# Optimization experiments

Measured on AMD Instinct MI355X. Metric: run time of the kernel, lower is better.

Reference implementation:

```python
import jax, jax.numpy as jnp
import numpy as np

SEQ_LEN = 1000
IN_DIM = 100
POOL = SEQ_LEN // IN_DIM  # 10
HIDDEN = 64
OUT_DIM = 5
N_BASIS = 16
BATCH = 65536


def setup_inputs() -> dict:
    key = jax.random.key(0)
    k1, k2, k3 = jax.random.split(key, 3)
    x = jax.random.normal(k1, (BATCH, SEQ_LEN), dtype=jnp.float32)
    c1_mu = jax.random.normal(k2, (HIDDEN, IN_DIM, N_BASIS), dtype=jnp.float32) * 0.05
    c2_mu = jax.random.normal(k3, (OUT_DIM, HIDDEN, N_BASIS), dtype=jnp.float32) * 0.05
    centers = jnp.linspace(-3.0, 3.0, N_BASIS, dtype=jnp.float32)
    return {"x": x, "c1_mu": c1_mu, "c2_mu": c2_mu, "centers": centers}


def _norm(x):
    # torch .std() uses ddof=1 (unbiased)
    mu = jnp.mean(x, axis=1, keepdims=True)
    sd = jnp.std(x, axis=1, keepdims=True, ddof=1)
    return (x - mu) / (sd + 1e-6)


def _basis(x, centers):
    # x: [b, d] -> [b, d, n_basis]; RBF with fixed variance 0.36
    d = x[..., None] - centers
    return jnp.exp(-0.5 * d * d / 0.36)


def _kan(x, c, centers):
    B = _basis(x, centers)  # [b, i, n]
    return jnp.einsum('bin,oin->bo', B, c)


def reference(x, c1_mu, c2_mu, centers):
    b = x.shape[0]
    # unfold(1, pool, pool).mean(-1): non-overlapping average pooling
    x = x.reshape(b, IN_DIM, POOL).mean(-1)  # [b, 100]
    x = _norm(x)
    h = jnp.tanh(_kan(x, c1_mu, centers))  # [b, 64]
    h = _norm(h)
    out = _kan(h, c2_mu, centers)  # [b, 5]
    return out
```

## Files before the change

### kernel.cpp

```cpp
#include <hip/hip_runtime.h>
#include <hip/hip_bf16.h>


#define SEQ    1000
#define INDIM  100
#define HID    64
#define OUTD   5
#define ROWS   16
#define NTHR   128

typedef __bf16 v8bf __attribute__((ext_vector_type(8)));
typedef float  v4f  __attribute__((ext_vector_type(4)));

#define XSTR 101
#define HSTR 65
#define RSTR 68
#define R2STR 20

#if __has_builtin(__builtin_amdgcn_exp2f)
#define EXP2(x) __builtin_amdgcn_exp2f(x)
#else
#define EXP2(x) exp2f(x)
#endif
#if __has_builtin(__builtin_amdgcn_rcpf)
#define RCP(x) __builtin_amdgcn_rcpf(x)
#else
#define RCP(x) (1.f / (x))
#endif
#if __has_builtin(__builtin_amdgcn_sqrtf)
#define SQRT(x) __builtin_amdgcn_sqrtf(x)
#else
#define SQRT(x) sqrtf(x)
#endif

__global__ __launch_bounds__(256) void cvt_w(
    const float* __restrict__ c1, const float* __restrict__ c2,
    __bf16* __restrict__ c1b, __bf16* __restrict__ c2b)
{
  int t = blockIdx.x * 256 + threadIdx.x;
  if (t < 25600) {
    float4 v = ((const float4*)c1)[t];
    __bf16* d = c1b + t * 4;
    d[0] = (__bf16)v.x; d[1] = (__bf16)v.y; d[2] = (__bf16)v.z; d[3] = (__bf16)v.w;
  }
  if (t < 4096) {
    int o = t >> 8;
    __bf16* d = c2b + t * 4;
    if (o < OUTD) {
      float4 v = ((const float4*)c2)[t];
      d[0] = (__bf16)v.x; d[1] = (__bf16)v.y; d[2] = (__bf16)v.z; d[3] = (__bf16)v.w;
    } else {
      d[0] = (__bf16)0.f; d[1] = (__bf16)0.f; d[2] = (__bf16)0.f; d[3] = (__bf16)0.f;
    }
  }
}

__global__ __launch_bounds__(NTHR, 8) void kan_main(
    const float* __restrict__ x, const __bf16* __restrict__ c1b,
    const __bf16* __restrict__ c2bw, const float* __restrict__ cen,
    float* __restrict__ out)
{
  __shared__ __align__(16) float sm[2128];
  float* xn   = sm;
  float* red  = sm;
  float* hb   = sm + 1088;
  float* red2 = sm;

  const int tid  = threadIdx.x;
  const int w    = tid >> 6, lane = tid & 63;
  const int row0 = blockIdx.x * ROWS;
  const int l15 = lane & 15, q = lane >> 4, iq = q >> 1;

  const float Sn2 = 1.41553628f;
  const float TL2 = 2.88539008f;
  float cs[8];
  {
    const int n0 = (q & 1) * 8;
    #pragma unroll
    for (int j = 0; j < 8; ++j) cs[j] = cen[n0 + j] * Sn2;
  }

  const int pr   = (w << 3) + (lane & 7);
  const int slot = lane >> 3;
  float pva[14];
  float s = 0.f, s2 = 0.f;
  {
    const float* xg = x + (size_t)(row0 + pr) * SEQ;
    #pragma unroll
    for (int it = 0; it < 7; ++it) {
      int p = slot + (it << 3);
      float u0 = 0.f, u1 = 0.f;
      if (p < 50) {
        const float4* xp = (const float4*)(xg + p * 20);
        float4 a0 = xp[0], a1 = xp[1], a2 = xp[2], a3 = xp[3], a4 = xp[4];
        u0 = a0.x+a0.y+a0.z+a0.w + a1.x+a1.y+a1.z+a1.w + a2.x+a2.y;
        u1 = a2.z+a2.w + a3.x+a3.y+a3.z+a3.w + a4.x+a4.y+a4.z+a4.w;
        s += u0 + u1; s2 += u0*u0 + u1*u1;
      }
      pva[2*it] = u0; pva[2*it+1] = u1;
    }
  }
  #pragma unroll
  for (int m = 8; m <= 32; m <<= 1) {
    s += __shfl_xor(s, m, 64); s2 += __shfl_xor(s2, m, 64);
  }
  {
    float mu  = s * 0.01f;
    float var = (s2 - 100.f * mu * mu) * (1.f / 99.f);
    float rs  = Sn2 * RCP(SQRT(fmaxf(var, 0.f)) + 1e-5f);
    #pragma unroll
    for (int it = 0; it < 7; ++it) {
      int p = slot + (it << 3);
      if (p < 50) {
        xn[pr * XSTR + 2*p]     = (pva[2*it]     - mu) * rs;
        xn[pr * XSTR + 2*p + 1] = (pva[2*it + 1] - mu) * rs;
      }
    }
  }
  __syncthreads();

  const float* xr = xn + l15 * XSTR;
  const __bf16* bq = c1b + q * 8;
  v4f acc[4];
  acc[0] = (v4f){0.f,0.f,0.f,0.f}; acc[1] = acc[0]; acc[2] = acc[0]; acc[3] = acc[0];

  #pragma unroll 2
  for (int c5 = 0; c5 < 5; ++c5) {
    int c = w * 5 + c5;
    #pragma unroll
    for (int ks = 0; ks < 5; ++ks) {
      float xv = xr[c * 10 + 2 * ks + iq];
      v8bf a;
      #pragma unroll
      for (int j = 0; j < 8; ++j) {
        float d = xv - cs[j];
        a[j] = (__bf16)EXP2(-(d * d));
      }
      int ko = c * 160 + ks * 32;
      #pragma unroll
      for (int cb = 0; cb < 4; ++cb) {
        v8bf b = *(const v8bf*)(bq + (size_t)(cb * 16 + l15) * 1600 + ko);
        acc[cb] = __builtin_amdgcn_mfma_f32_16x16x32_bf16(a, b, acc[cb], 0, 0, 0);
      }
    }
  }
  __syncthreads();

  #pragma unroll
  for (int rgo = 0; rgo < 2; ++rgo) {
    int rg = 2 * (1 - w) + rgo;
    #pragma unroll
    for (int cb = 0; cb < 4; ++cb)
      red[(q * 4 + rg) * RSTR + cb * 16 + l15] = acc[cb][rg];
  }
  __syncthreads();
  #pragma unroll
  for (int rgo = 0; rgo < 2; ++rgo) {
    int rg = 2 * w + rgo;
    float h[4], ss = 0.f, ss2 = 0.f;
    #pragma unroll
    for (int cb = 0; cb < 4; ++cb) {
      float t = acc[cb][rg] + red[(q * 4 + rg) * RSTR + cb * 16 + l15];
      float e = EXP2(t * TL2);
      float hv = 1.f - 2.f * RCP(e + 1.f);
      h[cb] = hv; ss += hv; ss2 += hv * hv;
    }
    #pragma unroll
    for (int m = 1; m <= 8; m <<= 1) {
      ss += __shfl_xor(ss, m, 64); ss2 += __shfl_xor(ss2, m, 64);
    }
    float muh  = ss * (1.f / 64.f);
    float varh = (ss2 - 64.f * muh * muh) * (1.f / 63.f);
    float rsh  = Sn2 * RCP(SQRT(fmaxf(varh, 0.f)) + 1e-6f);
    #pragma unroll
    for (int cb = 0; cb < 4; ++cb)
      hb[(q * 4 + rg) * HSTR + cb * 16 + l15] = (h[cb] - muh) * rsh;
  }
  __syncthreads();

  const float* hr = hb + l15 * HSTR;
  const __bf16* bq2 = c2bw + (size_t)l15 * 1024 + q * 8;
  v4f o4 = (v4f){0.f, 0.f, 0.f, 0.f};
  #pragma unroll 4
  for (int t = 0; t < 16; ++t) {
    int t8 = w * 16 + t;
    float hv = hr[2 * t8 + iq];
    v8bf a;
    #pragma unroll
    for (int j = 0; j < 8; ++j) {
      float d = hv - cs[j];
      a[j] = (__bf16)EXP2(-(d * d));
    }
    v8bf vb = *(const v8bf*)(bq2 + t8 * 32);
    o4 = __builtin_amdgcn_mfma_f32_16x16x32_bf16(a, vb, o4, 0, 0, 0);
  }
  if (w == 0) {
    #pragma unroll
    for (int rg = 0; rg < 4; ++rg)
      red2[(q * 4 + rg) * R2STR + l15] = o4[rg];
  }
  __syncthreads();
  if (w == 1 && l15 < OUTD) {
    #pragma unroll
    for (int rg = 0; rg < 4; ++rg) {
      int r = q * 4 + rg;
      out[(size_t)(row0 + r) * OUTD + l15] = o4[rg] + red2[r * R2STR + l15];
    }
  }
}

extern "C" void kernel_launch(void* const* d_in, const int* in_sizes, int n_in,
                              void* d_out, int out_size, void* d_ws, size_t ws_size,
                              hipStream_t stream) {
  const float* x   = (const float*)d_in[0];
  const float* c1  = (const float*)d_in[1];
  const float* c2  = (const float*)d_in[2];
  const float* cen = (const float*)d_in[3];
  float* out = (float*)d_out;

  __bf16* c1b = (__bf16*)d_ws;
  __bf16* c2b = (__bf16*)((char*)d_ws + 204800);

  hipLaunchKernelGGL(cvt_w, dim3(100), dim3(256), 0, stream, c1, c2, c1b, c2b);
  hipLaunchKernelGGL(kan_main, dim3(65536 / ROWS), dim3(NTHR), 0, stream,
                     x, c1b, c2b, cen, out);
}
```

Measured before the change: 451.8 us.

## Pre-pack weights into MFMA fragment order and software-pipeline B loads

The weight-conversion kernel now writes c1 and c2 in the per-lane MFMA B-fragment layout, so each lane reads one contiguous 16-byte chunk per fragment instead of strided rows. The main kernel double-buffers these B fragments in registers, prefetching the next step's weights while the current MFMAs run. It also fully unrolls the loops with hoisted x/h loads, and changes the pooling thread mapping so each row's partial sums reduce over adjacent lanes. In exchange it uses more registers, so the occupancy hint in launch bounds drops from 8 to 6.

```diff
diff --git a/kernel.cpp b/kernel.cpp
--- a/kernel.cpp
+++ b/kernel.cpp
@@ -35,29 +35,40 @@
 
 __global__ __launch_bounds__(256) void cvt_w(
     const float* __restrict__ c1, const float* __restrict__ c2,
-    __bf16* __restrict__ c1b, __bf16* __restrict__ c2b)
+    __bf16* __restrict__ c1p, __bf16* __restrict__ c2p)
 {
   int t = blockIdx.x * 256 + threadIdx.x;
-  if (t < 25600) {
-    float4 v = ((const float4*)c1)[t];
-    __bf16* d = c1b + t * 4;
-    d[0] = (__bf16)v.x; d[1] = (__bf16)v.y; d[2] = (__bf16)v.z; d[3] = (__bf16)v.w;
-  }
-  if (t < 4096) {
-    int o = t >> 8;
-    __bf16* d = c2b + t * 4;
-    if (o < OUTD) {
-      float4 v = ((const float4*)c2)[t];
-      d[0] = (__bf16)v.x; d[1] = (__bf16)v.y; d[2] = (__bf16)v.z; d[3] = (__bf16)v.w;
+  if (t < 12800) {
+    int lane = t & 63, frag = t >> 6;
+    int cb = frag & 3, ks = frag >> 2;
+    int l15 = lane & 15, q = lane >> 4;
+    const float4* s = (const float4*)(c1 + (size_t)(cb * 16 + l15) * 1600 + ks * 32 + q * 8);
+    float4 v0 = s[0], v1 = s[1];
+    __bf16* d = c1p + (size_t)t * 8;
+    d[0]=(__bf16)v0.x; d[1]=(__bf16)v0.y; d[2]=(__bf16)v0.z; d[3]=(__bf16)v0.w;
+    d[4]=(__bf16)v1.x; d[5]=(__bf16)v1.y; d[6]=(__bf16)v1.z; d[7]=(__bf16)v1.w;
+  }
+  if (t < 2048) {
+    int lane = t & 63, t8 = t >> 6;
+    int row = lane & 15, q = lane >> 4;
+    __bf16* d = c2p + (size_t)t * 8;
+    if (row < OUTD) {
+      const float4* s = (const float4*)(c2 + (size_t)row * 1024 + t8 * 32 + q * 8);
+      float4 v0 = s[0], v1 = s[1];
+      d[0]=(__bf16)v0.x; d[1]=(__bf16)v0.y; d[2]=(__bf16)v0.z; d[3]=(__bf16)v0.w;
+      d[4]=(__bf16)v1.x; d[5]=(__bf16)v1.y; d[6]=(__bf16)v1.z; d[7]=(__bf16)v1.w;
     } else {
-      d[0] = (__bf16)0.f; d[1] = (__bf16)0.f; d[2] = (__bf16)0.f; d[3] = (__bf16)0.f;
+      #pragma unroll
+      for (int j = 0; j < 8; ++j) d[j] = (__bf16)0.f;
     }
   }
 }
 
-__global__ __launch_bounds__(NTHR, 8) void kan_main(
-    const float* __restrict__ x, const __bf16* __restrict__ c1b,
-    const __bf16* __restrict__ c2bw, const float* __restrict__ cen,
+#define MFMA __builtin_amdgcn_mfma_f32_16x16x32_bf16
+
+__global__ __launch_bounds__(NTHR, 6) void kan_main(
+    const float* __restrict__ x, const __bf16* __restrict__ c1p,
+    const __bf16* __restrict__ c2p, const float* __restrict__ cen,
     float* __restrict__ out)
 {
   __shared__ __align__(16) float sm[2128];
@@ -80,8 +91,8 @@
     for (int j = 0; j < 8; ++j) cs[j] = cen[n0 + j] * Sn2;
   }
 
-  const int pr   = (w << 3) + (lane & 7);
-  const int slot = lane >> 3;
+  const int pr   = (w << 3) + (lane >> 3);
+  const int slot = lane & 7;
   float pva[14];
   float s = 0.f, s2 = 0.f;
   {
@@ -101,7 +112,7 @@
     }
   }
   #pragma unroll
-  for (int m = 8; m <= 32; m <<= 1) {
+  for (int m = 1; m <= 4; m <<= 1) {
     s += __shfl_xor(s, m, 64); s2 += __shfl_xor(s2, m, 64);
   }
   {
@@ -120,28 +131,46 @@
   __syncthreads();
 
   const float* xr = xn + l15 * XSTR;
-  const __bf16* bq = c1b + q * 8;
+  const __bf16* bp = c1p + (size_t)(51200 * w) + lane * 8;
   v4f acc[4];
   acc[0] = (v4f){0.f,0.f,0.f,0.f}; acc[1] = acc[0]; acc[2] = acc[0]; acc[3] = acc[0];
 
-  #pragma unroll 2
+  v8bf bA0 = *(const v8bf*)(bp +    0);
+  v8bf bA1 = *(const v8bf*)(bp +  512);
+  v8bf bA2 = *(const v8bf*)(bp + 1024);
+  v8bf bA3 = *(const v8bf*)(bp + 1536);
+  bp += 2048;
+
+  #pragma unroll
   for (int c5 = 0; c5 < 5; ++c5) {
-    int c = w * 5 + c5;
+    const int c = w * 5 + c5;
+    float xv[5];
+    #pragma unroll
+    for (int k = 0; k < 5; ++k) xv[k] = xr[c * 10 + 2 * k + iq];
     #pragma unroll
     for (int ks = 0; ks < 5; ++ks) {
-      float xv = xr[c * 10 + 2 * ks + iq];
+      v8bf nb0, nb1, nb2, nb3;
+      if (c5 * 5 + ks < 24) {
+        nb0 = *(const v8bf*)(bp +    0);
+        nb1 = *(const v8bf*)(bp +  512);
+        nb2 = *(const v8bf*)(bp + 1024);
+        nb3 = *(const v8bf*)(bp + 1536);
+      }
+      bp += 2048;
       v8bf a;
-      #pragma unroll
-      for (int j = 0; j < 8; ++j) {
-        float d = xv - cs[j];
-        a[j] = (__bf16)EXP2(-(d * d));
-      }
-      int ko = c * 160 + ks * 32;
-      #pragma unroll
-      for (int cb = 0; cb < 4; ++cb) {
-        v8bf b = *(const v8bf*)(bq + (size_t)(cb * 16 + l15) * 1600 + ko);
-        acc[cb] = __builtin_amdgcn_mfma_f32_16x16x32_bf16(a, b, acc[cb], 0, 0, 0);
-      }
+      {
+        float xvk = xv[ks];
+        #pragma unroll
+        for (int j = 0; j < 8; ++j) {
+          float d = xvk - cs[j];
+          a[j] = (__bf16)EXP2(-(d * d));
+        }
+      }
+      acc[0] = MFMA(a, bA0, acc[0], 0, 0, 0);
+      acc[1] = MFMA(a, bA1, acc[1], 0, 0, 0);
+      acc[2] = MFMA(a, bA2, acc[2], 0, 0, 0);
+      acc[3] = MFMA(a, bA3, acc[3], 0, 0, 0);
+      if (c5 * 5 + ks < 24) { bA0 = nb0; bA1 = nb1; bA2 = nb2; bA3 = nb3; }
     }
   }
   __syncthreads();
@@ -179,20 +208,27 @@
   __syncthreads();
 
   const float* hr = hb + l15 * HSTR;
-  const __bf16* bq2 = c2bw + (size_t)l15 * 1024 + q * 8;
+  float hv16[16];
+  #pragma unroll
+  for (int t = 0; t < 16; ++t) hv16[t] = hr[2 * (16 * w + t) + iq];
+  const __bf16* bp2 = c2p + (size_t)(16 * w) * 512 + lane * 8;
+  v8bf vb = *(const v8bf*)(bp2);
   v4f o4 = (v4f){0.f, 0.f, 0.f, 0.f};
-  #pragma unroll 4
+  #pragma unroll
   for (int t = 0; t < 16; ++t) {
-    int t8 = w * 16 + t;
-    float hv = hr[2 * t8 + iq];
+    v8bf nvb;
+    if (t < 15) nvb = *(const v8bf*)(bp2 + (t + 1) * 512);
     v8bf a;
-    #pragma unroll
-    for (int j = 0; j < 8; ++j) {
-      float d = hv - cs[j];
-      a[j] = (__bf16)EXP2(-(d * d));
-    }
-    v8bf vb = *(const v8bf*)(bq2 + t8 * 32);
-    o4 = __builtin_amdgcn_mfma_f32_16x16x32_bf16(a, vb, o4, 0, 0, 0);
+    {
+      float hvv = hv16[t];
+      #pragma unroll
+      for (int j = 0; j < 8; ++j) {
+        float d = hvv - cs[j];
+        a[j] = (__bf16)EXP2(-(d * d));
+      }
+    }
+    o4 = MFMA(a, vb, o4, 0, 0, 0);
+    if (t < 15) vb = nvb;
   }
   if (w == 0) {
     #pragma unroll
@@ -218,10 +254,10 @@
   const float* cen = (const float*)d_in[3];
   float* out = (float*)d_out;
 
-  __bf16* c1b = (__bf16*)d_ws;
-  __bf16* c2b = (__bf16*)((char*)d_ws + 204800);
-
-  hipLaunchKernelGGL(cvt_w, dim3(100), dim3(256), 0, stream, c1, c2, c1b, c2b);
+  __bf16* c1p = (__bf16*)d_ws;
+  __bf16* c2p = (__bf16*)((char*)d_ws + 204800);
+
+  hipLaunchKernelGGL(cvt_w, dim3(50), dim3(256), 0, stream, c1, c2, c1p, c2p);
   hipLaunchKernelGGL(kan_main, dim3(65536 / ROWS), dim3(NTHR), 0, stream,
-                     x, c1b, c2b, cen, out);
+                     x, c1p, c2p, cen, out);
 }
```

After: 401.0 us. 11.2% less time.
